# Optimization experiments

Hardware: AMD Instinct MI355X
Metric: run time of the kernel (lower is better)

The kernel has to match this reference:

```python
import jax, jax.numpy as jnp
import numpy as np

H, N, L, BATCH = 128, 64, 4096, 8


def _make_dplr_hippo(n):
    # HiPPO-LegS -> NPLR -> DPLR diagonalization (float64 numpy, as in torch source)
    ar = np.arange(n, dtype=np.float64)
    p0 = np.sqrt(1.0 + 2.0 * ar)
    A = p0[:, None] * p0[None, :]
    A = np.tril(A) - np.diag(ar)
    nhippo = -A
    Pv = np.sqrt(ar + 0.5)
    Bv = np.sqrt(2.0 * ar + 1.0)
    S = nhippo + Pv[:, None] * Pv[None, :]
    Lambda_real = np.mean(np.diag(S)) * np.ones(n)
    Lambda_imag, V = np.linalg.eigh(S * -1j)
    V = V.astype(np.complex64)
    P = (V.conj().T @ Pv.astype(np.complex64))
    B = (V.conj().T @ Bv.astype(np.complex64))
    Lam = (Lambda_real + 1j * Lambda_imag).astype(np.complex64)
    return Lam, P, B


def _ri(x):  # complex -> [..., 2] real view (like torch.view_as_real)
    return np.stack([x.real, x.imag], axis=-1).astype(np.float32)


def setup_inputs() -> dict:
    key = jax.random.key(0)
    k_u, k_c, k_d = jax.random.split(key, 3)
    Lam, P, B = _make_dplr_hippo(N)
    Lambda_ri = np.tile(_ri(Lam)[None], (H, 1, 1))          # [H, N, 2]
    P_ri = np.tile(_ri(P)[None], (H, 1, 1))                 # [H, N, 2]
    B_ri = np.tile(_ri(B)[None], (H, 1, 1))                 # [H, N, 2]
    C_ri = jax.random.normal(k_c, (H, N, 2), dtype=jnp.float32)
    D = jax.random.normal(k_d, (H, 1), dtype=jnp.float32)
    u = jax.random.normal(k_u, (BATCH, L, H), dtype=jnp.float32)
    step = jnp.array([1.0 / L], dtype=jnp.float32)
    return {
        "u": u,
        "B_ri": jnp.asarray(B_ri),
        "C_ri": jnp.asarray(C_ri),
        "D": D,
        "Lambda_ri": jnp.asarray(Lambda_ri),
        "P_ri": jnp.asarray(P_ri),
        "step": step,
    }


def _as_c(x_ri):
    return jax.lax.complex(x_ri[..., 0], x_ri[..., 1])


def reference(u, B_ri, C_ri, D, Lambda_ri, P_ri, step):
    Bc = _as_c(B_ri)        # [H, N] complex64
    Cc = _as_c(C_ri)        # [H, N]
    Lam = _as_c(Lambda_ri)  # [H, N]
    Pc = _as_c(P_ri)        # [H, N]
    batch, seq_len, h = u.shape

    # roots of unity and bilinear-transform terms
    z = jnp.exp(-2j * jnp.pi * jnp.arange(seq_len) / seq_len)   # [L] complex64
    g = (2.0 / step).astype(jnp.complex64) * ((1.0 - z) / (1.0 + z))  # [L]
    c = 2.0 / (1.0 + z)                                          # [L]

    # Cauchy resolvent, shared by the four cauchy_dot reductions: [H, L, N]
    r = 1.0 / (g[None, :, None] - Lam[:, None, :])

    def cauchy(v):  # v: [H, N] -> [H, L]
        return jnp.einsum("hn,hln->hl", v, r)

    k00 = cauchy(jnp.conj(Cc) * Bc)
    k01 = cauchy(jnp.conj(Cc) * Pc)
    k10 = cauchy(jnp.conj(Pc) * Bc)
    k11 = cauchy(jnp.conj(Pc) * Pc)
    at_roots = c[None, :] * (k00 - k01 * (1.0 / (1.0 + k11)) * k10)  # [H, L]

    kernel = jnp.fft.ifft(at_roots, n=seq_len, axis=-1).real  # [H, L] float32

    # linear (full) FFT convolution, length 2L-1, keep first L samples
    nfft = 2 * seq_len - 1
    u_f = jnp.fft.rfft(u, n=nfft, axis=1)                 # [B, F, H]
    k_f = jnp.fft.rfft(kernel, n=nfft, axis=-1)           # [H, F]
    y = jnp.fft.irfft(u_f * k_f.T[None], n=nfft, axis=1)[:, :seq_len, :]  # [B, L, H]

    return y + u @ D  # D: [H,1] -> broadcast add of skip term
```

## Files before the change

### kernel.cpp

```cpp
#include <hip/hip_runtime.h>
#include <hip/hip_bf16.h>
#include <hip/hip_fp16.h>
#include <math.h>

#define HH 128
#define NN 64
#define LL 4096
#define BB 8
#define NFFT 8192
#define KSTR 4160

#define CAU_BLOCKS 1024
#define TRU_BLOCKS 4096
#define SKP_BLOCKS 8192

__device__ __forceinline__ float2 cmul(float2 a, float2 b) {
    return make_float2(a.x * b.x - a.y * b.y, a.x * b.y + a.y * b.x);
}
__device__ __forceinline__ float2 cadd(float2 a, float2 b) {
    return make_float2(a.x + b.x, a.y + b.y);
}
__device__ __forceinline__ float2 csub(float2 a, float2 b) {
    return make_float2(a.x - b.x, a.y - b.y);
}
__device__ __forceinline__ int brev13(int x) { return (int)(__brev((unsigned)x) >> 19); }
__device__ __forceinline__ int kkmap(int t) {
    return (t < 4096) ? (((t & 63) << 6) | (t >> 6)) : 4096;
}
__device__ __forceinline__ int swz(int v) { return v ^ ((v >> 4) & 15); }

__device__ __forceinline__ float2 twid(float rev, float sg) {
    return make_float2(__builtin_amdgcn_cosf(rev), sg * __builtin_amdgcn_sinf(rev));
}


template <int M>
__device__ __forceinline__ void dif_f8(float2* d, int N, int tid, int nt, float sg) {
    const float inv2m = 1.0f / (2.0f * (float)M);
    const float inv4m = 1.0f / (4.0f * (float)M);
    const float inv8m = 1.0f / (8.0f * (float)M);
    const float s2 = 0.70710678118654752f;
    for (int q = tid; q < (N >> 3); q += nt) {
        int j = q & (M - 1);
        int i0 = ((q & ~(M - 1)) << 3) + j;
        float2 x0 = d[swz(i0)],         x1 = d[swz(i0 + M)],
               x2 = d[swz(i0 + 2 * M)], x3 = d[swz(i0 + 3 * M)],
               x4 = d[swz(i0 + 4 * M)], x5 = d[swz(i0 + 5 * M)],
               x6 = d[swz(i0 + 6 * M)], x7 = d[swz(i0 + 7 * M)];
        float jf = (float)j;
        float2 w8 = twid(jf * inv8m, sg);
        float2 w4 = twid(jf * inv4m, sg);
        float2 w2 = twid(jf * inv2m, sg);
        float2 e1 = make_float2(s2, sg * s2);
        float2 e3 = make_float2(-s2, sg * s2);
        float2 y0 = cadd(x0, x4), y1 = cadd(x1, x5), y2 = cadd(x2, x6), y3 = cadd(x3, x7);
        float2 t0 = csub(x0, x4), t1 = csub(x1, x5), t2 = csub(x2, x6), t3 = csub(x3, x7);
        float2 w8i = make_float2(-sg * w8.y, sg * w8.x);
        float2 z0 = cmul(w8, t0);
        float2 z1 = cmul(cmul(w8, e1), t1);
        float2 z2 = cmul(w8i, t2);
        float2 z3 = cmul(cmul(w8, e3), t3);
        {
            float2 a0 = cadd(y0, y2);
            float2 a2 = cmul(w4, csub(y0, y2));
            float2 a1 = cadd(y1, y3);
            float2 t = cmul(w4, csub(y1, y3));
            float2 a3 = make_float2(-sg * t.y, sg * t.x);
            d[swz(i0)]         = cadd(a0, a1);
            d[swz(i0 + M)]     = cmul(w2, csub(a0, a1));
            d[swz(i0 + 2 * M)] = cadd(a2, a3);
            d[swz(i0 + 3 * M)] = cmul(w2, csub(a2, a3));
        }
        {
            float2 a0 = cadd(z0, z2);
            float2 a2 = cmul(w4, csub(z0, z2));
            float2 a1 = cadd(z1, z3);
            float2 t = cmul(w4, csub(z1, z3));
            float2 a3 = make_float2(-sg * t.y, sg * t.x);
            d[swz(i0 + 4 * M)] = cadd(a0, a1);
            d[swz(i0 + 5 * M)] = cmul(w2, csub(a0, a1));
            d[swz(i0 + 6 * M)] = cadd(a2, a3);
            d[swz(i0 + 7 * M)] = cmul(w2, csub(a2, a3));
        }
    }
    __syncthreads();
}

template <int M>
__device__ __forceinline__ void dit_f8(float2* d, int N, int tid, int nt, float sg) {
    const float inv2m = 1.0f / (2.0f * (float)M);
    const float inv4m = 1.0f / (4.0f * (float)M);
    const float inv8m = 1.0f / (8.0f * (float)M);
    const float s2 = 0.70710678118654752f;
    for (int q = tid; q < (N >> 3); q += nt) {
        int j = q & (M - 1);
        int i0 = ((q & ~(M - 1)) << 3) + j;
        float2 x0 = d[swz(i0)],         x1 = d[swz(i0 + M)],
               x2 = d[swz(i0 + 2 * M)], x3 = d[swz(i0 + 3 * M)],
               x4 = d[swz(i0 + 4 * M)], x5 = d[swz(i0 + 5 * M)],
               x6 = d[swz(i0 + 6 * M)], x7 = d[swz(i0 + 7 * M)];
        float jf = (float)j;
        float2 wA = twid(jf * inv2m, sg);
        float2 wB = twid(jf * inv4m, sg);
        float2 wC = twid(jf * inv8m, sg);
        float2 t;
        t = cmul(wA, x1); float2 b0 = cadd(x0, t), b1 = csub(x0, t);
        t = cmul(wA, x3); float2 b2 = cadd(x2, t), b3 = csub(x2, t);
        t = cmul(wA, x5); float2 b4 = cadd(x4, t), b5 = csub(x4, t);
        t = cmul(wA, x7); float2 b6 = cadd(x6, t), b7 = csub(x6, t);
        float2 wBi = make_float2(-sg * wB.y, sg * wB.x);
        t = cmul(wB, b2);  float2 c0 = cadd(b0, t), c2 = csub(b0, t);
        t = cmul(wBi, b3); float2 c1 = cadd(b1, t), c3 = csub(b1, t);
        t = cmul(wB, b6);  float2 c4 = cadd(b4, t), c6 = csub(b4, t);
        t = cmul(wBi, b7); float2 c5 = cadd(b5, t), c7 = csub(b5, t);
        float2 e1 = make_float2(s2, sg * s2);
        float2 e3 = make_float2(-s2, sg * s2);
        float2 w1 = cmul(wC, e1);
        float2 w2_ = make_float2(-sg * wC.y, sg * wC.x);
        float2 w3 = cmul(wC, e3);
        t = cmul(wC, c4);  d[swz(i0)]         = cadd(c0, t); d[swz(i0 + 4 * M)] = csub(c0, t);
        t = cmul(w1, c5);  d[swz(i0 + M)]     = cadd(c1, t); d[swz(i0 + 5 * M)] = csub(c1, t);
        t = cmul(w2_, c6); d[swz(i0 + 2 * M)] = cadd(c2, t); d[swz(i0 + 6 * M)] = csub(c2, t);
        t = cmul(w3, c7);  d[swz(i0 + 3 * M)] = cadd(c3, t); d[swz(i0 + 7 * M)] = csub(c3, t);
    }
    __syncthreads();
}

__global__ __launch_bounds__(256, 8) void stage1_kernel(
    const float* __restrict__ u,
    const float* __restrict__ B_ri, const float* __restrict__ C_ri,
    const float* __restrict__ D,
    const float* __restrict__ Lambda_ri, const float* __restrict__ P_ri,
    const float* __restrict__ step,
    float2* __restrict__ at_g, float2* __restrict__ ut2, float* __restrict__ skip) {
    __shared__ float4 smem4[264];
    const int bid = blockIdx.x;
    const int tid = threadIdx.x;

    if (bid < CAU_BLOCKS) {
        float* v11f = (float*)(smem4 + 128);
        const int h = bid >> 3;
        if (tid < NN) {
            int n = tid;
            float2 C = ((const float2*)C_ri)[h * NN + n];
            float2 Bv = ((const float2*)B_ri)[h * NN + n];
            float2 P = ((const float2*)P_ri)[h * NN + n];
            float2 lam = ((const float2*)Lambda_ri)[h * NN + n];
            float2 Cc = make_float2(C.x, -C.y);
            float2 Pc = make_float2(P.x, -P.y);
            float2 v00 = cmul(Cc, Bv);
            float2 v01 = cmul(Cc, P);
            float2 v10 = cmul(Pc, Bv);
            smem4[2 * n + 0] = make_float4(lam.x, lam.y, v00.x, v00.y);
            smem4[2 * n + 1] = make_float4(v01.x, v01.y, v10.x, v10.y);
            v11f[n] = P.x * P.x + P.y * P.y;
        }
        __syncthreads();

        const int lbase = ((bid & 7) << 8) | tid;
        const float two_over_step = 2.0f / step[0];
        float gr[2], gi[2], ccx[2], ccy[2];
#pragma unroll
        for (int p = 0; p < 2; ++p) {
            int l = lbase + p * 2048;
            double th = -6.283185307179586476925286766559 * (double)l / (double)LL;
            float sn, cs;
            sincosf((float)th, &sn, &cs);
            float dr = 1.0f + cs, di = sn;
            float inv = __builtin_amdgcn_rcpf(dr * dr + di * di);
            float nr = 1.0f - cs, ni = -sn;
            gr[p] = two_over_step * (nr * dr + ni * di) * inv;
            gi[p] = two_over_step * (ni * dr - nr * di) * inv;
            ccx[p] = 2.0f * dr * inv;
            ccy[p] = -2.0f * di * inv;
        }

        float2 k00[2], k01[2], k10[2], k11[2];
#pragma unroll
        for (int p = 0; p < 2; ++p) {
            k00[p] = make_float2(0.f, 0.f);
            k01[p] = make_float2(0.f, 0.f);
            k10[p] = make_float2(0.f, 0.f);
            k11[p] = make_float2(0.f, 0.f);
        }
#pragma unroll 4
        for (int n = 0; n < NN; ++n) {
            float4 tA = smem4[2 * n + 0];
            float4 tB = smem4[2 * n + 1];
            float w11 = v11f[n];
#pragma unroll
            for (int p = 0; p < 2; ++p) {
                float ar = gr[p] - tA.x, ai = gi[p] - tA.y;
                float id = __builtin_amdgcn_rcpf(ar * ar + ai * ai);
                float2 r = make_float2(ar * id, -ai * id);
                k00[p] = cadd(k00[p], cmul(make_float2(tA.z, tA.w), r));
                k01[p] = cadd(k01[p], cmul(make_float2(tB.x, tB.y), r));
                k10[p] = cadd(k10[p], cmul(make_float2(tB.z, tB.w), r));
                k11[p].x += w11 * r.x;
                k11[p].y += w11 * r.y;
            }
        }
#pragma unroll
        for (int p = 0; p < 2; ++p) {
            float wr = 1.0f + k11[p].x, wi = k11[p].y;
            float iw = __builtin_amdgcn_rcpf(wr * wr + wi * wi);
            float2 winv = make_float2(wr * iw, -wi * iw);
            float2 t = cmul(cmul(k01[p], winv), k10[p]);
            float2 at = cmul(make_float2(ccx[p], ccy[p]),
                             make_float2(k00[p].x - t.x, k00[p].y - t.y));
            at_g[(size_t)h * LL + lbase + p * 2048] = at;
        }
    } else if (bid < CAU_BLOCKS + TRU_BLOCKS) {
        float* tile = (float*)smem4;
        int tb = bid - CAU_BLOCKS;
        int b = tb >> 9;
        int hq = (tb >> 7) & 3;
        int h0 = hq * 32;
        int l0 = (tb & 127) * 32;
        int tx = tid & 31, ty = tid >> 5;
        const float* up = u + (size_t)b * LL * HH;
        for (int i = ty; i < 32; i += 8)
            tile[i * 33 + tx] = up[(size_t)(l0 + i) * HH + h0 + tx];
        __syncthreads();
        float2* utp = ut2 + (size_t)b * 64 * LL;
#pragma unroll
        for (int i = ty; i < 16; i += 8) {
            int c = (h0 >> 1) + i;
            float2 v = make_float2(tile[tx * 33 + 2 * i], tile[tx * 33 + 2 * i + 1]);
            utp[(size_t)c * LL + l0 + tx] = v;
        }
    } else {
        int sb = bid - (CAU_BLOCKS + TRU_BLOCKS);
        int wid = tid >> 6, lane = tid & 63;
        int row = sb * 4 + wid;
        const float* ur = u + (size_t)row * HH;
        float v = ur[lane] * D[lane] + ur[lane + 64] * D[lane + 64];
        for (int off = 32; off > 0; off >>= 1) v += __shfl_down(v, off, 64);
        if (lane == 0) skip[row] = v;
    }
}

__global__ __launch_bounds__(1024) void kfreq_kernel(const float2* __restrict__ at_g,
                                                     float2* __restrict__ KfP) {
    __shared__ float2 sm[NFFT];
    const int h = blockIdx.x;
    const int tid = threadIdx.x;
    const float2* ap = at_g + (size_t)h * LL;
#pragma unroll
    for (int it = 0; it < 4; ++it) {
        int t = tid + it * 1024;
        int l = ((t & 63) << 6) | (t >> 6);
        sm[swz((int)(__brev((unsigned)l) >> 20))] = ap[l];
    }
    __syncthreads();

    dit_f8<1>(sm, 4096, tid, 1024, +1.f);
    dit_f8<8>(sm, 4096, tid, 1024, +1.f);
    dit_f8<64>(sm, 4096, tid, 1024, +1.f);
    dit_f8<512>(sm, 4096, tid, 1024, +1.f);

    const float inv8192 = 1.0f / 8192.0f;
    for (int t = tid; t < 4096; t += 1024) {
        float kv = sm[swz(t)].x * (1.0f / 4096.0f);
        float2 w = twid((float)t * inv8192, -1.f);
        sm[swz(t)] = make_float2(kv, 0.f);
        sm[swz(t + 4096)] = make_float2(kv * w.x, kv * w.y);
    }
    __syncthreads();

    dif_f8<512>(sm, 8192, tid, 1024, -1.f);
    dif_f8<64>(sm, 8192, tid, 1024, -1.f);
    dif_f8<8>(sm, 8192, tid, 1024, -1.f);
    dif_f8<1>(sm, 8192, tid, 1024, -1.f);

    float2* kfp = KfP + (size_t)h * KSTR;
    for (int t = tid; t <= 4096; t += 1024) kfp[t] = sm[swz(brev13(kkmap(t)))];
}

__global__ __launch_bounds__(1024) void conv_fft_kernel(const float2* __restrict__ ut2,
                                                        const float2* __restrict__ KfP,
                                                        __half2* __restrict__ yt2) {
    __shared__ float2 sm[NFFT];
    const int b = blockIdx.x >> 6;
    const int c = blockIdx.x & 63;
    const int h0 = 2 * c, h1 = 2 * c + 1;
    const int tid = threadIdx.x;
    const float2* up2 = ut2 + ((size_t)b * 64 + c) * LL;
    const float inv8192 = 1.0f / 8192.0f;

    for (int i = tid; i < 4096; i += 1024) {
        float2 a = up2[i];
        float2 w = twid((float)i * inv8192, -1.f);
        sm[swz(i)] = a;
        sm[swz(i + 4096)] = cmul(w, a);
    }
    __syncthreads();

    dif_f8<512>(sm, 8192, tid, 1024, -1.f);
    dif_f8<64>(sm, 8192, tid, 1024, -1.f);
    dif_f8<8>(sm, 8192, tid, 1024, -1.f);
    dif_f8<1>(sm, 8192, tid, 1024, -1.f);

    const float2* kf0 = KfP + (size_t)h0 * KSTR;
    const float2* kf1 = KfP + (size_t)h1 * KSTR;
    for (int t = tid; t <= 4096; t += 1024) {
        int kk = kkmap(t);
        bool self = (kk == 0) || (kk == 4096);
        int p = swz(brev13(kk));
        int q = self ? p : swz(brev13(NFFT - kk));
        float2 K0 = kf0[t];
        float2 K1 = kf1[t];
        float2 Zp = sm[p];
        float2 Zq = sm[q];
        float2 U0 = make_float2(0.5f * (Zp.x + Zq.x), 0.5f * (Zp.y - Zq.y));
        float2 U1 = make_float2(0.5f * (Zp.y + Zq.y), 0.5f * (Zq.x - Zp.x));
        float2 A = cmul(U0, K0);
        float2 C = cmul(U1, K1);
        sm[p] = make_float2(A.x - C.y, A.y + C.x);
        if (!self) sm[q] = make_float2(A.x + C.y, C.x - A.y);
    }
    __syncthreads();

    dit_f8<1>(sm, 8192, tid, 1024, +1.f);
    dit_f8<8>(sm, 8192, tid, 1024, +1.f);
    dit_f8<64>(sm, 8192, tid, 1024, +1.f);
    dit_f8<512>(sm, 8192, tid, 1024, +1.f);

    __half2* yp = yt2 + ((size_t)b * 64 + c) * LL;
    const float invN = 1.0f / (float)NFFT;
    for (int x = tid; x < 4096; x += 1024) {
        float2 w = twid((float)x * inv8192, +1.f);
        float2 a = sm[swz(x)];
        float2 bb = cmul(w, sm[swz(x + 4096)]);
        yp[x] = __floats2half2_rn((a.x + bb.x) * invN, (a.y + bb.y) * invN);
    }
}

__global__ __launch_bounds__(256) void transpose_y_kernel(const __half2* __restrict__ yt2,
                                                          const float* __restrict__ skip,
                                                          float* __restrict__ y) {
    __shared__ __half2 tile[32 * 17];
    int b = blockIdx.z;
    int c0 = blockIdx.x * 16;
    int l0 = blockIdx.y * 32;
    int tx = threadIdx.x, ty = threadIdx.y;
    const __half2* ytp = yt2 + (size_t)b * 64 * LL;
    const float* skp = skip + (size_t)b * LL;
    float* yp = y + (size_t)b * LL * HH;
    for (int i = ty; i < 16; i += 8)
        tile[tx * 17 + i] = ytp[(size_t)(c0 + i) * LL + l0 + tx];
    __syncthreads();
    int h0 = c0 * 2;
    for (int i = ty; i < 32; i += 8) {
        int l = l0 + i;
        float sk = skp[l];
        float2 f = __half22float2(tile[i * 17 + (tx >> 1)]);
        float v = (tx & 1) ? f.y : f.x;
        yp[(size_t)l * HH + h0 + tx] = v + sk;
    }
}

extern "C" void kernel_launch(void* const* d_in, const int* in_sizes, int n_in,
                              void* d_out, int out_size, void* d_ws, size_t ws_size,
                              hipStream_t stream) {
    const float* u = (const float*)d_in[0];
    const float* B_ri = (const float*)d_in[1];
    const float* C_ri = (const float*)d_in[2];
    const float* D = (const float*)d_in[3];
    const float* Lambda_ri = (const float*)d_in[4];
    const float* P_ri = (const float*)d_in[5];
    const float* step = (const float*)d_in[6];
    float* out = (float*)d_out;

    char* ws = (char*)d_ws;
    float2* KfP = (float2*)ws;
    float* skip = (float*)(ws + (size_t)6 * 1024 * 1024);
    float2* ut2 = (float2*)(ws + (size_t)8 * 1024 * 1024);
    char* hi = ws + (size_t)24 * 1024 * 1024;
    float2* at_g = (float2*)hi;
    __half2* yt2 = (__half2*)hi;

    stage1_kernel<<<dim3(CAU_BLOCKS + TRU_BLOCKS + SKP_BLOCKS), dim3(256), 0, stream>>>(
        u, B_ri, C_ri, D, Lambda_ri, P_ri, step, at_g, ut2, skip);
    kfreq_kernel<<<dim3(HH), dim3(1024), 0, stream>>>(at_g, KfP);
    conv_fft_kernel<<<dim3(BB * HH / 2), dim3(1024), 0, stream>>>(ut2, KfP, yt2);
    transpose_y_kernel<<<dim3(HH / 32, LL / 32, BB), dim3(32, 8), 0, stream>>>(yt2, skip, out);
}
```

Baseline: 79.52 us.

## Vectorize FFT shared-memory passes with paired float4 accesses and new swizzle

Result: no change. 80.66 us (+1.4%).

```diff
diff --git a/kernel.cpp b/kernel.cpp
--- a/kernel.cpp
+++ b/kernel.cpp
@@ -27,101 +27,175 @@
 __device__ __forceinline__ int kkmap(int t) {
     return (t < 4096) ? (((t & 63) << 6) | (t >> 6)) : 4096;
 }
-__device__ __forceinline__ int swz(int v) { return v ^ ((v >> 4) & 15); }
+__device__ __forceinline__ int psw(int pv) { return pv ^ ((pv >> 3) & 7); }
+__device__ __forceinline__ int slotf(int v) { return (psw(v >> 1) << 1) | (v & 1); }
 
 __device__ __forceinline__ float2 twid(float rev, float sg) {
     return make_float2(__builtin_amdgcn_cosf(rev), sg * __builtin_amdgcn_sinf(rev));
 }
 
 
+__device__ __forceinline__ void bfly8_dif(float2 x[8], float jf, float inv2m,
+                                          float inv4m, float inv8m, float sg) {
+    const float s2 = 0.70710678118654752f;
+    float2 w8 = twid(jf * inv8m, sg);
+    float2 w4 = twid(jf * inv4m, sg);
+    float2 w2 = twid(jf * inv2m, sg);
+    float2 e1 = make_float2(s2, sg * s2);
+    float2 e3 = make_float2(-s2, sg * s2);
+    float2 y0 = cadd(x[0], x[4]), y1 = cadd(x[1], x[5]);
+    float2 y2 = cadd(x[2], x[6]), y3 = cadd(x[3], x[7]);
+    float2 t0 = csub(x[0], x[4]), t1 = csub(x[1], x[5]);
+    float2 t2 = csub(x[2], x[6]), t3 = csub(x[3], x[7]);
+    float2 w8i = make_float2(-sg * w8.y, sg * w8.x);
+    float2 z0 = cmul(w8, t0);
+    float2 z1 = cmul(cmul(w8, e1), t1);
+    float2 z2 = cmul(w8i, t2);
+    float2 z3 = cmul(cmul(w8, e3), t3);
+    {
+        float2 a0 = cadd(y0, y2);
+        float2 a2 = cmul(w4, csub(y0, y2));
+        float2 a1 = cadd(y1, y3);
+        float2 t = cmul(w4, csub(y1, y3));
+        float2 a3 = make_float2(-sg * t.y, sg * t.x);
+        x[0] = cadd(a0, a1);
+        x[1] = cmul(w2, csub(a0, a1));
+        x[2] = cadd(a2, a3);
+        x[3] = cmul(w2, csub(a2, a3));
+    }
+    {
+        float2 a0 = cadd(z0, z2);
+        float2 a2 = cmul(w4, csub(z0, z2));
+        float2 a1 = cadd(z1, z3);
+        float2 t = cmul(w4, csub(z1, z3));
+        float2 a3 = make_float2(-sg * t.y, sg * t.x);
+        x[4] = cadd(a0, a1);
+        x[5] = cmul(w2, csub(a0, a1));
+        x[6] = cadd(a2, a3);
+        x[7] = cmul(w2, csub(a2, a3));
+    }
+}
+
+__device__ __forceinline__ void bfly8_dit(float2 x[8], float jf, float inv2m,
+                                          float inv4m, float inv8m, float sg) {
+    const float s2 = 0.70710678118654752f;
+    float2 wA = twid(jf * inv2m, sg);
+    float2 wB = twid(jf * inv4m, sg);
+    float2 wC = twid(jf * inv8m, sg);
+    float2 t;
+    t = cmul(wA, x[1]); float2 b0 = cadd(x[0], t), b1 = csub(x[0], t);
+    t = cmul(wA, x[3]); float2 b2 = cadd(x[2], t), b3 = csub(x[2], t);
+    t = cmul(wA, x[5]); float2 b4 = cadd(x[4], t), b5 = csub(x[4], t);
+    t = cmul(wA, x[7]); float2 b6 = cadd(x[6], t), b7 = csub(x[6], t);
+    float2 wBi = make_float2(-sg * wB.y, sg * wB.x);
+    t = cmul(wB, b2);  float2 c0 = cadd(b0, t), c2 = csub(b0, t);
+    t = cmul(wBi, b3); float2 c1 = cadd(b1, t), c3 = csub(b1, t);
+    t = cmul(wB, b6);  float2 c4 = cadd(b4, t), c6 = csub(b4, t);
+    t = cmul(wBi, b7); float2 c5 = cadd(b5, t), c7 = csub(b5, t);
+    float2 e1 = make_float2(s2, sg * s2);
+    float2 e3 = make_float2(-s2, sg * s2);
+    float2 w1 = cmul(wC, e1);
+    float2 w2_ = make_float2(-sg * wC.y, sg * wC.x);
+    float2 w3 = cmul(wC, e3);
+    t = cmul(wC, c4);  x[0] = cadd(c0, t); x[4] = csub(c0, t);
+    t = cmul(w1, c5);  x[1] = cadd(c1, t); x[5] = csub(c1, t);
+    t = cmul(w2_, c6); x[2] = cadd(c2, t); x[6] = csub(c2, t);
+    t = cmul(w3, c7);  x[3] = cadd(c3, t); x[7] = csub(c3, t);
+}
+
+
 template <int M>
-__device__ __forceinline__ void dif_f8(float2* d, int N, int tid, int nt, float sg) {
+__device__ __forceinline__ void dif_f8p(float2* d, int N, int tid, int nt, float sg) {
     const float inv2m = 1.0f / (2.0f * (float)M);
     const float inv4m = 1.0f / (4.0f * (float)M);
     const float inv8m = 1.0f / (8.0f * (float)M);
-    const float s2 = 0.70710678118654752f;
-    for (int q = tid; q < (N >> 3); q += nt) {
-        int j = q & (M - 1);
-        int i0 = ((q & ~(M - 1)) << 3) + j;
-        float2 x0 = d[swz(i0)],         x1 = d[swz(i0 + M)],
-               x2 = d[swz(i0 + 2 * M)], x3 = d[swz(i0 + 3 * M)],
-               x4 = d[swz(i0 + 4 * M)], x5 = d[swz(i0 + 5 * M)],
-               x6 = d[swz(i0 + 6 * M)], x7 = d[swz(i0 + 7 * M)];
-        float jf = (float)j;
-        float2 w8 = twid(jf * inv8m, sg);
-        float2 w4 = twid(jf * inv4m, sg);
-        float2 w2 = twid(jf * inv2m, sg);
-        float2 e1 = make_float2(s2, sg * s2);
-        float2 e3 = make_float2(-s2, sg * s2);
-        float2 y0 = cadd(x0, x4), y1 = cadd(x1, x5), y2 = cadd(x2, x6), y3 = cadd(x3, x7);
-        float2 t0 = csub(x0, x4), t1 = csub(x1, x5), t2 = csub(x2, x6), t3 = csub(x3, x7);
-        float2 w8i = make_float2(-sg * w8.y, sg * w8.x);
-        float2 z0 = cmul(w8, t0);
-        float2 z1 = cmul(cmul(w8, e1), t1);
-        float2 z2 = cmul(w8i, t2);
-        float2 z3 = cmul(cmul(w8, e3), t3);
-        {
-            float2 a0 = cadd(y0, y2);
-            float2 a2 = cmul(w4, csub(y0, y2));
-            float2 a1 = cadd(y1, y3);
-            float2 t = cmul(w4, csub(y1, y3));
-            float2 a3 = make_float2(-sg * t.y, sg * t.x);
-            d[swz(i0)]         = cadd(a0, a1);
-            d[swz(i0 + M)]     = cmul(w2, csub(a0, a1));
-            d[swz(i0 + 2 * M)] = cadd(a2, a3);
-            d[swz(i0 + 3 * M)] = cmul(w2, csub(a2, a3));
-        }
-        {
-            float2 a0 = cadd(z0, z2);
-            float2 a2 = cmul(w4, csub(z0, z2));
-            float2 a1 = cadd(z1, z3);
-            float2 t = cmul(w4, csub(z1, z3));
-            float2 a3 = make_float2(-sg * t.y, sg * t.x);
-            d[swz(i0 + 4 * M)] = cadd(a0, a1);
-            d[swz(i0 + 5 * M)] = cmul(w2, csub(a0, a1));
-            d[swz(i0 + 6 * M)] = cadd(a2, a3);
-            d[swz(i0 + 7 * M)] = cmul(w2, csub(a2, a3));
-        }
+    for (int s = tid; s < (N >> 4); s += nt) {
+        int jp = s & (M / 2 - 1);
+        int i0 = ((s & ~(M / 2 - 1)) << 4) + 2 * jp;
+        int pv0 = i0 >> 1;
+        int adr[8];
+        float2 lo[8], hi[8];
+#pragma unroll
+        for (int k = 0; k < 8; ++k) {
+            adr[k] = psw(pv0 + k * (M / 2)) << 1;
+            float4 v = *(const float4*)&d[adr[k]];
+            lo[k] = make_float2(v.x, v.y);
+            hi[k] = make_float2(v.z, v.w);
+        }
+        float jf = (float)(2 * jp);
+        bfly8_dif(lo, jf, inv2m, inv4m, inv8m, sg);
+        bfly8_dif(hi, jf + 1.0f, inv2m, inv4m, inv8m, sg);
+#pragma unroll
+        for (int k = 0; k < 8; ++k)
+            *(float4*)&d[adr[k]] = make_float4(lo[k].x, lo[k].y, hi[k].x, hi[k].y);
     }
     __syncthreads();
 }
 
 template <int M>
-__device__ __forceinline__ void dit_f8(float2* d, int N, int tid, int nt, float sg) {
+__device__ __forceinline__ void dit_f8p(float2* d, int N, int tid, int nt, float sg) {
     const float inv2m = 1.0f / (2.0f * (float)M);
     const float inv4m = 1.0f / (4.0f * (float)M);
     const float inv8m = 1.0f / (8.0f * (float)M);
-    const float s2 = 0.70710678118654752f;
+    for (int s = tid; s < (N >> 4); s += nt) {
+        int jp = s & (M / 2 - 1);
+        int i0 = ((s & ~(M / 2 - 1)) << 4) + 2 * jp;
+        int pv0 = i0 >> 1;
+        int adr[8];
+        float2 lo[8], hi[8];
+#pragma unroll
+        for (int k = 0; k < 8; ++k) {
+            adr[k] = psw(pv0 + k * (M / 2)) << 1;
+            float4 v = *(const float4*)&d[adr[k]];
+            lo[k] = make_float2(v.x, v.y);
+            hi[k] = make_float2(v.z, v.w);
+        }
+        float jf = (float)(2 * jp);
+        bfly8_dit(lo, jf, inv2m, inv4m, inv8m, sg);
+        bfly8_dit(hi, jf + 1.0f, inv2m, inv4m, inv8m, sg);
+#pragma unroll
+        for (int k = 0; k < 8; ++k)
+            *(float4*)&d[adr[k]] = make_float4(lo[k].x, lo[k].y, hi[k].x, hi[k].y);
+    }
+    __syncthreads();
+}
+
+__device__ __forceinline__ void dif_f8_m1(float2* d, int N, int tid, int nt, float sg) {
     for (int q = tid; q < (N >> 3); q += nt) {
-        int j = q & (M - 1);
-        int i0 = ((q & ~(M - 1)) << 3) + j;
-        float2 x0 = d[swz(i0)],         x1 = d[swz(i0 + M)],
-               x2 = d[swz(i0 + 2 * M)], x3 = d[swz(i0 + 3 * M)],
-               x4 = d[swz(i0 + 4 * M)], x5 = d[swz(i0 + 5 * M)],
-               x6 = d[swz(i0 + 6 * M)], x7 = d[swz(i0 + 7 * M)];
-        float jf = (float)j;
-        float2 wA = twid(jf * inv2m, sg);
-        float2 wB = twid(jf * inv4m, sg);
-        float2 wC = twid(jf * inv8m, sg);
-        float2 t;
-        t = cmul(wA, x1); float2 b0 = cadd(x0, t), b1 = csub(x0, t);
-        t = cmul(wA, x3); float2 b2 = cadd(x2, t), b3 = csub(x2, t);
-        t = cmul(wA, x5); float2 b4 = cadd(x4, t), b5 = csub(x4, t);
-        t = cmul(wA, x7); float2 b6 = cadd(x6, t), b7 = csub(x6, t);
-        float2 wBi = make_float2(-sg * wB.y, sg * wB.x);
-        t = cmul(wB, b2);  float2 c0 = cadd(b0, t), c2 = csub(b0, t);
-        t = cmul(wBi, b3); float2 c1 = cadd(b1, t), c3 = csub(b1, t);
-        t = cmul(wB, b6);  float2 c4 = cadd(b4, t), c6 = csub(b4, t);
-        t = cmul(wBi, b7); float2 c5 = cadd(b5, t), c7 = csub(b5, t);
-        float2 e1 = make_float2(s2, sg * s2);
-        float2 e3 = make_float2(-s2, sg * s2);
-        float2 w1 = cmul(wC, e1);
-        float2 w2_ = make_float2(-sg * wC.y, sg * wC.x);
-        float2 w3 = cmul(wC, e3);
-        t = cmul(wC, c4);  d[swz(i0)]         = cadd(c0, t); d[swz(i0 + 4 * M)] = csub(c0, t);
-        t = cmul(w1, c5);  d[swz(i0 + M)]     = cadd(c1, t); d[swz(i0 + 5 * M)] = csub(c1, t);
-        t = cmul(w2_, c6); d[swz(i0 + 2 * M)] = cadd(c2, t); d[swz(i0 + 6 * M)] = csub(c2, t);
-        t = cmul(w3, c7);  d[swz(i0 + 3 * M)] = cadd(c3, t); d[swz(i0 + 7 * M)] = csub(c3, t);
+        int pv0 = q << 2;
+        int adr[4];
+        float2 x[8];
+#pragma unroll
+        for (int k = 0; k < 4; ++k) {
+            adr[k] = psw(pv0 + k) << 1;
+            float4 v = *(const float4*)&d[adr[k]];
+            x[2 * k] = make_float2(v.x, v.y);
+            x[2 * k + 1] = make_float2(v.z, v.w);
+        }
+        bfly8_dif(x, 0.0f, 0.5f, 0.25f, 0.125f, sg);
+#pragma unroll
+        for (int k = 0; k < 4; ++k)
+            *(float4*)&d[adr[k]] = make_float4(x[2 * k].x, x[2 * k].y, x[2 * k + 1].x, x[2 * k + 1].y);
+    }
+    __syncthreads();
+}
+
+__device__ __forceinline__ void dit_f8_m1(float2* d, int N, int tid, int nt, float sg) {
+    for (int q = tid; q < (N >> 3); q += nt) {
+        int pv0 = q << 2;
+        int adr[4];
+        float2 x[8];
+#pragma unroll
+        for (int k = 0; k < 4; ++k) {
+            adr[k] = psw(pv0 + k) << 1;
+            float4 v = *(const float4*)&d[adr[k]];
+            x[2 * k] = make_float2(v.x, v.y);
+            x[2 * k + 1] = make_float2(v.z, v.w);
+        }
+        bfly8_dit(x, 0.0f, 0.5f, 0.25f, 0.125f, sg);
+#pragma unroll
+        for (int k = 0; k < 4; ++k)
+            *(float4*)&d[adr[k]] = make_float4(x[2 * k].x, x[2 * k].y, x[2 * k + 1].x, x[2 * k + 1].y);
     }
     __syncthreads();
 }
@@ -240,46 +314,46 @@
     }
 }
 
-__global__ __launch_bounds__(1024) void kfreq_kernel(const float2* __restrict__ at_g,
-                                                     float2* __restrict__ KfP) {
+__global__ __launch_bounds__(512) void kfreq_kernel(const float2* __restrict__ at_g,
+                                                    float2* __restrict__ KfP) {
     __shared__ float2 sm[NFFT];
     const int h = blockIdx.x;
     const int tid = threadIdx.x;
     const float2* ap = at_g + (size_t)h * LL;
 #pragma unroll
-    for (int it = 0; it < 4; ++it) {
-        int t = tid + it * 1024;
+    for (int it = 0; it < 8; ++it) {
+        int t = tid + it * 512;
         int l = ((t & 63) << 6) | (t >> 6);
-        sm[swz((int)(__brev((unsigned)l) >> 20))] = ap[l];
-    }
-    __syncthreads();
-
-    dit_f8<1>(sm, 4096, tid, 1024, +1.f);
-    dit_f8<8>(sm, 4096, tid, 1024, +1.f);
-    dit_f8<64>(sm, 4096, tid, 1024, +1.f);
-    dit_f8<512>(sm, 4096, tid, 1024, +1.f);
+        sm[slotf((int)(__brev((unsigned)l) >> 20))] = ap[l];
+    }
+    __syncthreads();
+
+    dit_f8_m1(sm, 4096, tid, 512, +1.f);
+    dit_f8p<8>(sm, 4096, tid, 512, +1.f);
+    dit_f8p<64>(sm, 4096, tid, 512, +1.f);
+    dit_f8p<512>(sm, 4096, tid, 512, +1.f);
 
     const float inv8192 = 1.0f / 8192.0f;
-    for (int t = tid; t < 4096; t += 1024) {
-        float kv = sm[swz(t)].x * (1.0f / 4096.0f);
+    for (int t = tid; t < 4096; t += 512) {
+        float kv = sm[slotf(t)].x * (1.0f / 4096.0f);
         float2 w = twid((float)t * inv8192, -1.f);
-        sm[swz(t)] = make_float2(kv, 0.f);
-        sm[swz(t + 4096)] = make_float2(kv * w.x, kv * w.y);
-    }
-    __syncthreads();
-
-    dif_f8<512>(sm, 8192, tid, 1024, -1.f);
-    dif_f8<64>(sm, 8192, tid, 1024, -1.f);
-    dif_f8<8>(sm, 8192, tid, 1024, -1.f);
-    dif_f8<1>(sm, 8192, tid, 1024, -1.f);
+        sm[slotf(t)] = make_float2(kv, 0.f);
+        sm[slotf(t + 4096)] = make_float2(kv * w.x, kv * w.y);
+    }
+    __syncthreads();
+
+    dif_f8p<512>(sm, 8192, tid, 512, -1.f);
+    dif_f8p<64>(sm, 8192, tid, 512, -1.f);
+    dif_f8p<8>(sm, 8192, tid, 512, -1.f);
+    dif_f8_m1(sm, 8192, tid, 512, -1.f);
 
     float2* kfp = KfP + (size_t)h * KSTR;
-    for (int t = tid; t <= 4096; t += 1024) kfp[t] = sm[swz(brev13(kkmap(t)))];
-}
-
-__global__ __launch_bounds__(1024) void conv_fft_kernel(const float2* __restrict__ ut2,
-                                                        const float2* __restrict__ KfP,
-                                                        __half2* __restrict__ yt2) {
+    for (int t = tid; t <= 4096; t += 512) kfp[t] = sm[slotf(brev13(kkmap(t)))];
+}
+
+__global__ __launch_bounds__(512) void conv_fft_kernel(const float2* __restrict__ ut2,
+                                                       const float2* __restrict__ KfP,
+                                                       __half2* __restrict__ yt2) {
     __shared__ float2 sm[NFFT];
     const int b = blockIdx.x >> 6;
     const int c = blockIdx.x & 63;
@@ -288,26 +362,30 @@
     const float2* up2 = ut2 + ((size_t)b * 64 + c) * LL;
     const float inv8192 = 1.0f / 8192.0f;
 
-    for (int i = tid; i < 4096; i += 1024) {
-        float2 a = up2[i];
-        float2 w = twid((float)i * inv8192, -1.f);
-        sm[swz(i)] = a;
-        sm[swz(i + 4096)] = cmul(w, a);
-    }
-    __syncthreads();
-
-    dif_f8<512>(sm, 8192, tid, 1024, -1.f);
-    dif_f8<64>(sm, 8192, tid, 1024, -1.f);
-    dif_f8<8>(sm, 8192, tid, 1024, -1.f);
-    dif_f8<1>(sm, 8192, tid, 1024, -1.f);
+    for (int x2 = tid; x2 < 2048; x2 += 512) {
+        int x = x2 << 1;
+        float4 a = *(const float4*)&up2[x];
+        float2 a0 = make_float2(a.x, a.y), a1 = make_float2(a.z, a.w);
+        float2 w0 = twid((float)x * inv8192, -1.f);
+        float2 w1 = twid((float)(x + 1) * inv8192, -1.f);
+        *(float4*)&sm[psw(x2) << 1] = a;
+        float2 c0 = cmul(w0, a0), c1 = cmul(w1, a1);
+        *(float4*)&sm[psw(x2 + 2048) << 1] = make_float4(c0.x, c0.y, c1.x, c1.y);
+    }
+    __syncthreads();
+
+    dif_f8p<512>(sm, 8192, tid, 512, -1.f);
+    dif_f8p<64>(sm, 8192, tid, 512, -1.f);
+    dif_f8p<8>(sm, 8192, tid, 512, -1.f);
+    dif_f8_m1(sm, 8192, tid, 512, -1.f);
 
     const float2* kf0 = KfP + (size_t)h0 * KSTR;
     const float2* kf1 = KfP + (size_t)h1 * KSTR;
-    for (int t = tid; t <= 4096; t += 1024) {
+    for (int t = tid; t <= 4096; t += 512) {
         int kk = kkmap(t);
         bool self = (kk == 0) || (kk == 4096);
-        int p = swz(brev13(kk));
-        int q = self ? p : swz(brev13(NFFT - kk));
+        int p = slotf(brev13(kk));
+        int q = self ? p : slotf(brev13(NFFT - kk));
         float2 K0 = kf0[t];
         float2 K1 = kf1[t];
         float2 Zp = sm[p];
@@ -321,18 +399,23 @@
     }
     __syncthreads();
 
-    dit_f8<1>(sm, 8192, tid, 1024, +1.f);
-    dit_f8<8>(sm, 8192, tid, 1024, +1.f);
-    dit_f8<64>(sm, 8192, tid, 1024, +1.f);
-    dit_f8<512>(sm, 8192, tid, 1024, +1.f);
+    dit_f8_m1(sm, 8192, tid, 512, +1.f);
+    dit_f8p<8>(sm, 8192, tid, 512, +1.f);
+    dit_f8p<64>(sm, 8192, tid, 512, +1.f);
+    dit_f8p<512>(sm, 8192, tid, 512, +1.f);
 
     __half2* yp = yt2 + ((size_t)b * 64 + c) * LL;
     const float invN = 1.0f / (float)NFFT;
-    for (int x = tid; x < 4096; x += 1024) {
-        float2 w = twid((float)x * inv8192, +1.f);
-        float2 a = sm[swz(x)];
-        float2 bb = cmul(w, sm[swz(x + 4096)]);
-        yp[x] = __floats2half2_rn((a.x + bb.x) * invN, (a.y + bb.y) * invN);
+    for (int x2 = tid; x2 < 2048; x2 += 512) {
+        int x = x2 << 1;
+        float4 a4 = *(const float4*)&sm[psw(x2) << 1];
+        float4 b4 = *(const float4*)&sm[psw(x2 + 2048) << 1];
+        float2 w0 = twid((float)x * inv8192, +1.f);
+        float2 w1 = twid((float)(x + 1) * inv8192, +1.f);
+        float2 bb0 = cmul(w0, make_float2(b4.x, b4.y));
+        float2 bb1 = cmul(w1, make_float2(b4.z, b4.w));
+        yp[x] = __floats2half2_rn((a4.x + bb0.x) * invN, (a4.y + bb0.y) * invN);
+        yp[x + 1] = __floats2half2_rn((a4.z + bb1.x) * invN, (a4.w + bb1.y) * invN);
     }
 }
 
@@ -382,7 +465,7 @@
 
     stage1_kernel<<<dim3(CAU_BLOCKS + TRU_BLOCKS + SKP_BLOCKS), dim3(256), 0, stream>>>(
         u, B_ri, C_ri, D, Lambda_ri, P_ri, step, at_g, ut2, skip);
-    kfreq_kernel<<<dim3(HH), dim3(1024), 0, stream>>>(at_g, KfP);
-    conv_fft_kernel<<<dim3(BB * HH / 2), dim3(1024), 0, stream>>>(ut2, KfP, yt2);
+    kfreq_kernel<<<dim3(HH), dim3(512), 0, stream>>>(at_g, KfP);
+    conv_fft_kernel<<<dim3(BB * HH / 2), dim3(512), 0, stream>>>(ut2, KfP, yt2);
     transpose_y_kernel<<<dim3(HH / 32, LL / 32, BB), dim3(32, 8), 0, stream>>>(yt2, skip, out);
 }
```

## Fuse last DIF radix-8 stage, spectrum multiply, and first DIT stage in registers

Applied to the files above, without the earlier changes.

Measured after the change: 90.84 us. 14.2% more time.

```diff
diff --git a/kernel.cpp b/kernel.cpp
--- a/kernel.cpp
+++ b/kernel.cpp
@@ -24,13 +24,106 @@
     return make_float2(a.x - b.x, a.y - b.y);
 }
 __device__ __forceinline__ int brev13(int x) { return (int)(__brev((unsigned)x) >> 19); }
-__device__ __forceinline__ int kkmap(int t) {
-    return (t < 4096) ? (((t & 63) << 6) | (t >> 6)) : 4096;
-}
+__device__ __forceinline__ int brev10(int x) { return (int)(__brev((unsigned)x) >> 22); }
 __device__ __forceinline__ int swz(int v) { return v ^ ((v >> 4) & 15); }
+
+__device__ __forceinline__ int k_of_slot(int s) {
+    if (s >= 4096) return 3584;
+    int t = s >> 3, j = s & 7;
+    if (t == 0) {
+        const int tab[8] = {0, 1024, 2048, 3072, 4096, 512, 1536, 2560};
+        return tab[j];
+    }
+    return (j < 4) ? j * 1024 + t : (j - 4) * 1024 + 1024 - t;
+}
 
 __device__ __forceinline__ float2 twid(float rev, float sg) {
     return make_float2(__builtin_amdgcn_cosf(rev), sg * __builtin_amdgcn_sinf(rev));
+}
+
+
+__device__ __forceinline__ void bfly8_dif(float2 x[8], float jf, float inv2m,
+                                          float inv4m, float inv8m, float sg) {
+    const float s2 = 0.70710678118654752f;
+    float2 w8 = twid(jf * inv8m, sg);
+    float2 w4 = twid(jf * inv4m, sg);
+    float2 w2 = twid(jf * inv2m, sg);
+    float2 e1 = make_float2(s2, sg * s2);
+    float2 e3 = make_float2(-s2, sg * s2);
+    float2 y0 = cadd(x[0], x[4]), y1 = cadd(x[1], x[5]);
+    float2 y2 = cadd(x[2], x[6]), y3 = cadd(x[3], x[7]);
+    float2 t0 = csub(x[0], x[4]), t1 = csub(x[1], x[5]);
+    float2 t2 = csub(x[2], x[6]), t3 = csub(x[3], x[7]);
+    float2 w8i = make_float2(-sg * w8.y, sg * w8.x);
+    float2 z0 = cmul(w8, t0);
+    float2 z1 = cmul(cmul(w8, e1), t1);
+    float2 z2 = cmul(w8i, t2);
+    float2 z3 = cmul(cmul(w8, e3), t3);
+    {
+        float2 a0 = cadd(y0, y2);
+        float2 a2 = cmul(w4, csub(y0, y2));
+        float2 a1 = cadd(y1, y3);
+        float2 t = cmul(w4, csub(y1, y3));
+        float2 a3 = make_float2(-sg * t.y, sg * t.x);
+        x[0] = cadd(a0, a1);
+        x[1] = cmul(w2, csub(a0, a1));
+        x[2] = cadd(a2, a3);
+        x[3] = cmul(w2, csub(a2, a3));
+    }
+    {
+        float2 a0 = cadd(z0, z2);
+        float2 a2 = cmul(w4, csub(z0, z2));
+        float2 a1 = cadd(z1, z3);
+        float2 t = cmul(w4, csub(z1, z3));
+        float2 a3 = make_float2(-sg * t.y, sg * t.x);
+        x[4] = cadd(a0, a1);
+        x[5] = cmul(w2, csub(a0, a1));
+        x[6] = cadd(a2, a3);
+        x[7] = cmul(w2, csub(a2, a3));
+    }
+}
+
+__device__ __forceinline__ void bfly8_dit(float2 x[8], float jf, float inv2m,
+                                          float inv4m, float inv8m, float sg) {
+    const float s2 = 0.70710678118654752f;
+    float2 wA = twid(jf * inv2m, sg);
+    float2 wB = twid(jf * inv4m, sg);
+    float2 wC = twid(jf * inv8m, sg);
+    float2 t;
+    t = cmul(wA, x[1]); float2 b0 = cadd(x[0], t), b1 = csub(x[0], t);
+    t = cmul(wA, x[3]); float2 b2 = cadd(x[2], t), b3 = csub(x[2], t);
+    t = cmul(wA, x[5]); float2 b4 = cadd(x[4], t), b5 = csub(x[4], t);
+    t = cmul(wA, x[7]); float2 b6 = cadd(x[6], t), b7 = csub(x[6], t);
+    float2 wBi = make_float2(-sg * wB.y, sg * wB.x);
+    t = cmul(wB, b2);  float2 c0 = cadd(b0, t), c2 = csub(b0, t);
+    t = cmul(wBi, b3); float2 c1 = cadd(b1, t), c3 = csub(b1, t);
+    t = cmul(wB, b6);  float2 c4 = cadd(b4, t), c6 = csub(b4, t);
+    t = cmul(wBi, b7); float2 c5 = cadd(b5, t), c7 = csub(b5, t);
+    float2 e1 = make_float2(s2, sg * s2);
+    float2 e3 = make_float2(-s2, sg * s2);
+    float2 w1 = cmul(wC, e1);
+    float2 w2_ = make_float2(-sg * wC.y, sg * wC.x);
+    float2 w3 = cmul(wC, e3);
+    t = cmul(wC, c4);  x[0] = cadd(c0, t); x[4] = csub(c0, t);
+    t = cmul(w1, c5);  x[1] = cadd(c1, t); x[5] = csub(c1, t);
+    t = cmul(w2_, c6); x[2] = cadd(c2, t); x[6] = csub(c2, t);
+    t = cmul(w3, c7);  x[3] = cadd(c3, t); x[7] = csub(c3, t);
+}
+
+__device__ __forceinline__ void pairpt(float2& P, float2& Q, float2 K0, float2 K1) {
+    float2 U0 = make_float2(0.5f * (P.x + Q.x), 0.5f * (P.y - Q.y));
+    float2 U1 = make_float2(0.5f * (P.y + Q.y), 0.5f * (Q.x - P.x));
+    float2 A = cmul(U0, K0);
+    float2 C = cmul(U1, K1);
+    P = make_float2(A.x - C.y, A.y + C.x);
+    Q = make_float2(A.x + C.y, C.x - A.y);
+}
+__device__ __forceinline__ void selfpt(float2& P, float2 K0, float2 K1) {
+    float2 U0 = make_float2(P.x, 0.f);
+    float2 U1 = make_float2(P.y, 0.f);
+    float2 A = cmul(U0, K0);
+    float2 C = cmul(U1, K1);
+    P = make_float2(A.x - C.y, A.y + C.x);
 }
 
 
@@ -39,49 +132,15 @@
     const float inv2m = 1.0f / (2.0f * (float)M);
     const float inv4m = 1.0f / (4.0f * (float)M);
     const float inv8m = 1.0f / (8.0f * (float)M);
-    const float s2 = 0.70710678118654752f;
     for (int q = tid; q < (N >> 3); q += nt) {
         int j = q & (M - 1);
         int i0 = ((q & ~(M - 1)) << 3) + j;
-        float2 x0 = d[swz(i0)],         x1 = d[swz(i0 + M)],
-               x2 = d[swz(i0 + 2 * M)], x3 = d[swz(i0 + 3 * M)],
-               x4 = d[swz(i0 + 4 * M)], x5 = d[swz(i0 + 5 * M)],
-               x6 = d[swz(i0 + 6 * M)], x7 = d[swz(i0 + 7 * M)];
-        float jf = (float)j;
-        float2 w8 = twid(jf * inv8m, sg);
-        float2 w4 = twid(jf * inv4m, sg);
-        float2 w2 = twid(jf * inv2m, sg);
-        float2 e1 = make_float2(s2, sg * s2);
-        float2 e3 = make_float2(-s2, sg * s2);
-        float2 y0 = cadd(x0, x4), y1 = cadd(x1, x5), y2 = cadd(x2, x6), y3 = cadd(x3, x7);
-        float2 t0 = csub(x0, x4), t1 = csub(x1, x5), t2 = csub(x2, x6), t3 = csub(x3, x7);
-        float2 w8i = make_float2(-sg * w8.y, sg * w8.x);
-        float2 z0 = cmul(w8, t0);
-        float2 z1 = cmul(cmul(w8, e1), t1);
-        float2 z2 = cmul(w8i, t2);
-        float2 z3 = cmul(cmul(w8, e3), t3);
-        {
-            float2 a0 = cadd(y0, y2);
-            float2 a2 = cmul(w4, csub(y0, y2));
-            float2 a1 = cadd(y1, y3);
-            float2 t = cmul(w4, csub(y1, y3));
-            float2 a3 = make_float2(-sg * t.y, sg * t.x);
-            d[swz(i0)]         = cadd(a0, a1);
-            d[swz(i0 + M)]     = cmul(w2, csub(a0, a1));
-            d[swz(i0 + 2 * M)] = cadd(a2, a3);
-            d[swz(i0 + 3 * M)] = cmul(w2, csub(a2, a3));
-        }
-        {
-            float2 a0 = cadd(z0, z2);
-            float2 a2 = cmul(w4, csub(z0, z2));
-            float2 a1 = cadd(z1, z3);
-            float2 t = cmul(w4, csub(z1, z3));
-            float2 a3 = make_float2(-sg * t.y, sg * t.x);
-            d[swz(i0 + 4 * M)] = cadd(a0, a1);
-            d[swz(i0 + 5 * M)] = cmul(w2, csub(a0, a1));
-            d[swz(i0 + 6 * M)] = cadd(a2, a3);
-            d[swz(i0 + 7 * M)] = cmul(w2, csub(a2, a3));
-        }
+        float2 x[8];
+#pragma unroll
+        for (int k = 0; k < 8; ++k) x[k] = d[swz(i0 + k * M)];
+        bfly8_dif(x, (float)j, inv2m, inv4m, inv8m, sg);
+#pragma unroll
+        for (int k = 0; k < 8; ++k) d[swz(i0 + k * M)] = x[k];
     }
     __syncthreads();
 }
@@ -91,37 +150,15 @@
     const float inv2m = 1.0f / (2.0f * (float)M);
     const float inv4m = 1.0f / (4.0f * (float)M);
     const float inv8m = 1.0f / (8.0f * (float)M);
-    const float s2 = 0.70710678118654752f;
     for (int q = tid; q < (N >> 3); q += nt) {
         int j = q & (M - 1);
         int i0 = ((q & ~(M - 1)) << 3) + j;
-        float2 x0 = d[swz(i0)],         x1 = d[swz(i0 + M)],
-               x2 = d[swz(i0 + 2 * M)], x3 = d[swz(i0 + 3 * M)],
-               x4 = d[swz(i0 + 4 * M)], x5 = d[swz(i0 + 5 * M)],
-               x6 = d[swz(i0 + 6 * M)], x7 = d[swz(i0 + 7 * M)];
-        float jf = (float)j;
-        float2 wA = twid(jf * inv2m, sg);
-        float2 wB = twid(jf * inv4m, sg);
-        float2 wC = twid(jf * inv8m, sg);
-        float2 t;
-        t = cmul(wA, x1); float2 b0 = cadd(x0, t), b1 = csub(x0, t);
-        t = cmul(wA, x3); float2 b2 = cadd(x2, t), b3 = csub(x2, t);
-        t = cmul(wA, x5); float2 b4 = cadd(x4, t), b5 = csub(x4, t);
-        t = cmul(wA, x7); float2 b6 = cadd(x6, t), b7 = csub(x6, t);
-        float2 wBi = make_float2(-sg * wB.y, sg * wB.x);
-        t = cmul(wB, b2);  float2 c0 = cadd(b0, t), c2 = csub(b0, t);
-        t = cmul(wBi, b3); float2 c1 = cadd(b1, t), c3 = csub(b1, t);
-        t = cmul(wB, b6);  float2 c4 = cadd(b4, t), c6 = csub(b4, t);
-        t = cmul(wBi, b7); float2 c5 = cadd(b5, t), c7 = csub(b5, t);
-        float2 e1 = make_float2(s2, sg * s2);
-        float2 e3 = make_float2(-s2, sg * s2);
-        float2 w1 = cmul(wC, e1);
-        float2 w2_ = make_float2(-sg * wC.y, sg * wC.x);
-        float2 w3 = cmul(wC, e3);
-        t = cmul(wC, c4);  d[swz(i0)]         = cadd(c0, t); d[swz(i0 + 4 * M)] = csub(c0, t);
-        t = cmul(w1, c5);  d[swz(i0 + M)]     = cadd(c1, t); d[swz(i0 + 5 * M)] = csub(c1, t);
-        t = cmul(w2_, c6); d[swz(i0 + 2 * M)] = cadd(c2, t); d[swz(i0 + 6 * M)] = csub(c2, t);
-        t = cmul(w3, c7);  d[swz(i0 + 3 * M)] = cadd(c3, t); d[swz(i0 + 7 * M)] = csub(c3, t);
+        float2 x[8];
+#pragma unroll
+        for (int k = 0; k < 8; ++k) x[k] = d[swz(i0 + k * M)];
+        bfly8_dit(x, (float)j, inv2m, inv4m, inv8m, sg);
+#pragma unroll
+        for (int k = 0; k < 8; ++k) d[swz(i0 + k * M)] = x[k];
     }
     __syncthreads();
 }
@@ -274,12 +311,13 @@
     dif_f8<1>(sm, 8192, tid, 1024, -1.f);
 
     float2* kfp = KfP + (size_t)h * KSTR;
-    for (int t = tid; t <= 4096; t += 1024) kfp[t] = sm[swz(brev13(kkmap(t)))];
-}
-
-__global__ __launch_bounds__(1024) void conv_fft_kernel(const float2* __restrict__ ut2,
-                                                        const float2* __restrict__ KfP,
-                                                        __half2* __restrict__ yt2) {
+    for (int s = tid; s <= 4096; s += 1024)
+        kfp[s] = sm[swz(brev13(k_of_slot(s)))];
+}
+
+__global__ __launch_bounds__(512) void conv_fft_kernel(const float2* __restrict__ ut2,
+                                                       const float2* __restrict__ KfP,
+                                                       __half2* __restrict__ yt2) {
     __shared__ float2 sm[NFFT];
     const int b = blockIdx.x >> 6;
     const int c = blockIdx.x & 63;
@@ -288,7 +326,7 @@
     const float2* up2 = ut2 + ((size_t)b * 64 + c) * LL;
     const float inv8192 = 1.0f / 8192.0f;
 
-    for (int i = tid; i < 4096; i += 1024) {
+    for (int i = tid; i < 4096; i += 512) {
         float2 a = up2[i];
         float2 w = twid((float)i * inv8192, -1.f);
         sm[swz(i)] = a;
@@ -296,39 +334,75 @@
     }
     __syncthreads();
 
-    dif_f8<512>(sm, 8192, tid, 1024, -1.f);
-    dif_f8<64>(sm, 8192, tid, 1024, -1.f);
-    dif_f8<8>(sm, 8192, tid, 1024, -1.f);
-    dif_f8<1>(sm, 8192, tid, 1024, -1.f);
-
-    const float2* kf0 = KfP + (size_t)h0 * KSTR;
-    const float2* kf1 = KfP + (size_t)h1 * KSTR;
-    for (int t = tid; t <= 4096; t += 1024) {
-        int kk = kkmap(t);
-        bool self = (kk == 0) || (kk == 4096);
-        int p = swz(brev13(kk));
-        int q = self ? p : swz(brev13(NFFT - kk));
-        float2 K0 = kf0[t];
-        float2 K1 = kf1[t];
-        float2 Zp = sm[p];
-        float2 Zq = sm[q];
-        float2 U0 = make_float2(0.5f * (Zp.x + Zq.x), 0.5f * (Zp.y - Zq.y));
-        float2 U1 = make_float2(0.5f * (Zp.y + Zq.y), 0.5f * (Zq.x - Zp.x));
-        float2 A = cmul(U0, K0);
-        float2 C = cmul(U1, K1);
-        sm[p] = make_float2(A.x - C.y, A.y + C.x);
-        if (!self) sm[q] = make_float2(A.x + C.y, C.x - A.y);
-    }
-    __syncthreads();
-
-    dit_f8<1>(sm, 8192, tid, 1024, +1.f);
-    dit_f8<8>(sm, 8192, tid, 1024, +1.f);
-    dit_f8<64>(sm, 8192, tid, 1024, +1.f);
-    dit_f8<512>(sm, 8192, tid, 1024, +1.f);
+    dif_f8<512>(sm, 8192, tid, 512, -1.f);
+    dif_f8<64>(sm, 8192, tid, 512, -1.f);
+    dif_f8<8>(sm, 8192, tid, 512, -1.f);
+
+    {
+        const int m = tid;
+        const int qa = (m == 0) ? 0 : brev10(m);
+        const int qb = (m == 0) ? 1 : brev10(1024 - m);
+        float2 xa[8], xb[8];
+#pragma unroll
+        for (int j = 0; j < 8; ++j) {
+            xa[j] = sm[swz(8 * qa + j)];
+            xb[j] = sm[swz(8 * qb + j)];
+        }
+        bfly8_dif(xa, 0.f, 0.5f, 0.25f, 0.125f, -1.f);
+        bfly8_dif(xb, 0.f, 0.5f, 0.25f, 0.125f, -1.f);
+
+        const float2* kf0 = KfP + (size_t)h0 * KSTR;
+        const float2* kf1 = KfP + (size_t)h1 * KSTR;
+        float2 K0[8], K1[8];
+        {
+            const float4* a4 = (const float4*)(kf0 + 8 * m);
+            const float4* b4 = (const float4*)(kf1 + 8 * m);
+#pragma unroll
+            for (int s = 0; s < 4; ++s) {
+                float4 v0 = a4[s], v1 = b4[s];
+                K0[2 * s] = make_float2(v0.x, v0.y);
+                K0[2 * s + 1] = make_float2(v0.z, v0.w);
+                K1[2 * s] = make_float2(v1.x, v1.y);
+                K1[2 * s + 1] = make_float2(v1.z, v1.w);
+            }
+        }
+        if (m == 0) {
+            selfpt(xa[0], K0[0], K1[0]);
+            pairpt(xa[4], xa[7], K0[1], K1[1]);
+            pairpt(xa[2], xa[3], K0[2], K1[2]);
+            pairpt(xa[6], xa[5], K0[3], K1[3]);
+            selfpt(xa[1], K0[4], K1[4]);
+            pairpt(xb[0], xb[7], K0[5], K1[5]);
+            pairpt(xb[4], xb[3], K0[6], K1[6]);
+            pairpt(xb[2], xb[5], K0[7], K1[7]);
+            pairpt(xb[6], xb[1], kf0[4096], kf1[4096]);
+        } else {
+            pairpt(xa[0], xb[7], K0[0], K1[0]);
+            pairpt(xa[4], xb[3], K0[1], K1[1]);
+            pairpt(xa[2], xb[5], K0[2], K1[2]);
+            pairpt(xa[6], xb[1], K0[3], K1[3]);
+            pairpt(xb[0], xa[7], K0[4], K1[4]);
+            pairpt(xb[4], xa[3], K0[5], K1[5]);
+            pairpt(xb[2], xa[5], K0[6], K1[6]);
+            pairpt(xb[6], xa[1], K0[7], K1[7]);
+        }
+        bfly8_dit(xa, 0.f, 0.5f, 0.25f, 0.125f, +1.f);
+        bfly8_dit(xb, 0.f, 0.5f, 0.25f, 0.125f, +1.f);
+#pragma unroll
+        for (int j = 0; j < 8; ++j) {
+            sm[swz(8 * qa + j)] = xa[j];
+            sm[swz(8 * qb + j)] = xb[j];
+        }
+    }
+    __syncthreads();
+
+    dit_f8<8>(sm, 8192, tid, 512, +1.f);
+    dit_f8<64>(sm, 8192, tid, 512, +1.f);
+    dit_f8<512>(sm, 8192, tid, 512, +1.f);
 
     __half2* yp = yt2 + ((size_t)b * 64 + c) * LL;
     const float invN = 1.0f / (float)NFFT;
-    for (int x = tid; x < 4096; x += 1024) {
+    for (int x = tid; x < 4096; x += 512) {
         float2 w = twid((float)x * inv8192, +1.f);
         float2 a = sm[swz(x)];
         float2 bb = cmul(w, sm[swz(x + 4096)]);
@@ -383,6 +457,6 @@
     stage1_kernel<<<dim3(CAU_BLOCKS + TRU_BLOCKS + SKP_BLOCKS), dim3(256), 0, stream>>>(
         u, B_ri, C_ri, D, Lambda_ri, P_ri, step, at_g, ut2, skip);
     kfreq_kernel<<<dim3(HH), dim3(1024), 0, stream>>>(at_g, KfP);
-    conv_fft_kernel<<<dim3(BB * HH / 2), dim3(1024), 0, stream>>>(ut2, KfP, yt2);
+    conv_fft_kernel<<<dim3(BB * HH / 2), dim3(512), 0, stream>>>(ut2, KfP, yt2);
     transpose_y_kernel<<<dim3(HH / 32, LL / 32, BB), dim3(32, 8), 0, stream>>>(yt2, skip, out);
 }
```
